# Kernel optimization log

Measured on AMD Instinct MI355X. Metric: run time of the kernel, lower is better.

The kernel has to match this reference:

```python
import jax, jax.numpy as jnp
import numpy as np

B, S, D = 2, 4096, 2048
H, DK = 16, 128          # num_heads, head_dim (DK == DV)
GATE_NORM = 16.0         # gate_logit_normalizer (GLA default)


def setup_inputs() -> dict:
    key = jax.random.key(0)
    ks = jax.random.split(key, 6)
    sc = 1.0 / np.sqrt(D)
    return {
        "x": jax.random.normal(ks[0], (B, S, D), dtype=jnp.float32),
        "Wq": jax.random.normal(ks[1], (D, D), dtype=jnp.float32) * sc,
        "Wk": jax.random.normal(ks[2], (D, D), dtype=jnp.float32) * sc,
        "Wv": jax.random.normal(ks[3], (D, D), dtype=jnp.float32) * sc,
        "Wg": jax.random.normal(ks[4], (D, D), dtype=jnp.float32) * sc,
        "Wo": jax.random.normal(ks[5], (D, D), dtype=jnp.float32) * sc,
    }


def _gla(q, k, v, gk):
    """Gated linear attention recurrence.
    q,k,gk: [B,H,S,DK]; v: [B,H,S,DV]. Returns o: [B,H,S,DV].
    S_t = diag(exp(gk_t)) @ S_{t-1} + k_t v_t^T;  o_t = q_t @ S_t.
    """
    def step(state, inp):
        q_t, k_t, v_t, g_t = inp  # each [B,H,DK] / [B,H,DV]
        state = state * jnp.exp(g_t)[..., None] + k_t[..., None] * v_t[..., None, :]
        o_t = jnp.einsum("bhk,bhkv->bhv", q_t, state)
        return state, o_t

    init = jnp.zeros((q.shape[0], q.shape[1], q.shape[3], v.shape[3]), q.dtype)
    # scan over time: move seq axis to front
    xs = tuple(jnp.moveaxis(t, 2, 0) for t in (q, k, v, gk))
    _, o = jax.lax.scan(step, init, xs)  # o: [S,B,H,DV]
    return jnp.moveaxis(o, 0, 2)


def reference(x, Wq, Wk, Wv, Wg, Wo):
    b, s, _ = x.shape
    split = lambda t: t.reshape(b, s, H, DK).transpose(0, 2, 1, 3)  # [B,H,S,DK]
    q = split(x @ Wq) * (DK ** -0.5)
    k = split(x @ Wk)
    v = split(x @ Wv)
    gk = jax.nn.log_sigmoid(split(x @ Wg)) / GATE_NORM  # data-dependent log decay
    o = _gla(q, k, v, gk)                                # [B,H,S,DV]
    o = o.transpose(0, 2, 1, 3).reshape(b, s, H * DK)
    return o @ Wo
```

## Files before the change

### kernel.cpp

```cpp
#include <hip/hip_runtime.h>
#include <hip/hip_bf16.h>

#define B_SZ 2
#define S_LEN 4096
#define D_MODEL 2048
#define NH 16
#define DKH 128
#define CHUNK 32
#define SEG 256
#define NSEG 16
#define NCH 8
#define GEMM_M 8192
#define GEMM_N 2048
#define GEMM_K 2048
#define NKT 32

typedef __bf16 bf16x8 __attribute__((ext_vector_type(8)));
typedef float f32x4 __attribute__((ext_vector_type(4)));
typedef unsigned short u16x4 __attribute__((ext_vector_type(4)));
typedef unsigned short u16x8 __attribute__((ext_vector_type(8)));

__device__ inline float bf2f(unsigned short u) {
  unsigned int x = ((unsigned int)u) << 16;
  return __builtin_bit_cast(float, x);
}
__device__ inline unsigned short f2bf(float f) {
  __hip_bfloat16 h = __float2bfloat16(f);
  return __builtin_bit_cast(unsigned short, h);
}
__device__ inline unsigned int packhl(float s) {
  unsigned short h = f2bf(s);
  unsigned short l = f2bf(s - bf2f(h));
  return ((unsigned int)h << 16) | (unsigned int)l;
}

__global__ __launch_bounds__(256) void cast_bf16_kernel(const float* __restrict__ in,
                                                        unsigned short* __restrict__ out,
                                                        int nvec8) {
  int i = blockIdx.x * 256 + threadIdx.x;
  if (i >= nvec8) return;
  const float4* p = (const float4*)in + (size_t)i * 2;
  float4 a = p[0], b = p[1];
  uint4 o;
  o.x = (unsigned)f2bf(a.x) | ((unsigned)f2bf(a.y) << 16);
  o.y = (unsigned)f2bf(a.z) | ((unsigned)f2bf(a.w) << 16);
  o.z = (unsigned)f2bf(b.x) | ((unsigned)f2bf(b.y) << 16);
  o.w = (unsigned)f2bf(b.z) | ((unsigned)f2bf(b.w) << 16);
  ((uint4*)out)[i] = o;
}

__global__ __launch_bounds__(256) void transpose_cast_kernel(const float* __restrict__ W,
                                                             unsigned short* __restrict__ Wt) {
  __shared__ float tile[64][65];
  const int n0 = blockIdx.x * 64, k0 = blockIdx.y * 64;
  for (int jj = 0; jj < 16; ++jj) {
    int flat = threadIdx.x + jj * 256;
    int r = flat >> 6, c = flat & 63;
    tile[r][c] = W[(size_t)(k0 + r) * D_MODEL + n0 + c];
  }
  __syncthreads();
  for (int jj = 0; jj < 16; ++jj) {
    int flat = threadIdx.x + jj * 256;
    int rr = flat >> 6, cc = flat & 63;
    Wt[(size_t)(n0 + rr) * D_MODEL + k0 + cc] = f2bf(tile[cc][rr]);
  }
}

__device__ __forceinline__ void async16(void* lds_dst, const void* gsrc) {
  __builtin_amdgcn_global_load_lds((__attribute__((address_space(1))) void*)(void*)gsrc,
                                   (__attribute__((address_space(3))) void*)lds_dst,
                                   16, 0, 0);
}

__device__ __forceinline__ void memfence_compiler() { asm volatile("" ::: "memory"); }

__device__ __forceinline__ void stage_tile(const unsigned short* __restrict__ G,
                                           int row0, int k0,
                                           unsigned short* lds_buf, int tid) {
  const int r = tid >> 3;
  const int ssw = ((tid & 7) ^ (r & 7)) * 8;
  const unsigned short* src = &G[(size_t)(row0 + r) * GEMM_K + k0 + ssw];
  char* dst = (char*)lds_buf + (tid >> 6) * 1024;
#pragma unroll
  for (int j = 0; j < 4; ++j)
    async16(dst + j * 8192, src + (size_t)j * 64 * GEMM_K);
}

template <int MODE>
__global__ __launch_bounds__(512, 2) void gemm256(const unsigned short* __restrict__ A,
                                                  const unsigned short* __restrict__ Bt,
                                                  void* __restrict__ Cout) {
  __shared__ unsigned short As[2][256 * 64];
  __shared__ unsigned short Bs[2][256 * 64];
  const int tid = threadIdx.x;
  const int lane = tid & 63;
  const int wid = tid >> 6;
  const int wm = wid >> 2, wn = wid & 3;
  const int lr = lane & 15, lg = lane >> 4;

  const int lid = blockIdx.y * 8 + blockIdx.x;
  const int swz = (lid & 7) * 32 + (lid >> 3);
  const int bm = (swz >> 3) * 256;
  const int bn = (swz & 7) * 256;

  f32x4 acc[8][4] = {};

  stage_tile(A, bm, 0, As[0], tid);
  stage_tile(Bt, bn, 0, Bs[0], tid);
  stage_tile(A, bm, 64, As[1], tid);
  stage_tile(Bt, bn, 64, Bs[1], tid);
  asm volatile("s_waitcnt vmcnt(8)" ::: "memory");
  __builtin_amdgcn_s_barrier();
  __builtin_amdgcn_sched_barrier(0);
  memfence_compiler();

  for (int t = 0; t < NKT; ++t) {
    const int cur = t & 1;
    const unsigned short* Ac = As[cur];
    const unsigned short* Bc = Bs[cur];
#pragma unroll
    for (int ks = 0; ks < 2; ++ks) {
      bf16x8 av[8], bv[4];
      const int slot = ((ks << 2) | lg) ^ (lr & 7);
#pragma unroll
      for (int mi = 0; mi < 8; ++mi)
        av[mi] = *(const bf16x8*)&Ac[(wm * 128 + mi * 16 + lr) * 64 + slot * 8];
#pragma unroll
      for (int nj = 0; nj < 4; ++nj)
        bv[nj] = *(const bf16x8*)&Bc[(wn * 64 + nj * 16 + lr) * 64 + slot * 8];
      __builtin_amdgcn_s_setprio(1);
#pragma unroll
      for (int mi = 0; mi < 8; ++mi)
#pragma unroll
        for (int nj = 0; nj < 4; ++nj)
          acc[mi][nj] = __builtin_amdgcn_mfma_f32_16x16x32_bf16(av[mi], bv[nj], acc[mi][nj], 0, 0, 0);
      __builtin_amdgcn_s_setprio(0);
    }
    memfence_compiler();
    __builtin_amdgcn_s_barrier();
    __builtin_amdgcn_sched_barrier(0);
    if (t + 2 < NKT) {
      stage_tile(A, bm, (t + 2) * 64, As[cur], tid);
      stage_tile(Bt, bn, (t + 2) * 64, Bs[cur], tid);
      asm volatile("s_waitcnt vmcnt(8)" ::: "memory");
    } else {
      asm volatile("s_waitcnt vmcnt(0)" ::: "memory");
    }
    __builtin_amdgcn_s_barrier();
    __builtin_amdgcn_sched_barrier(0);
    memfence_compiler();
  }

#pragma unroll
  for (int mi = 0; mi < 8; ++mi) {
#pragma unroll
    for (int nj = 0; nj < 4; ++nj) {
#pragma unroll
      for (int r = 0; r < 4; ++r) {
        int row = bm + wm * 128 + mi * 16 + lg * 4 + r;
        int col = bn + wn * 64 + nj * 16 + lr;
        float v = acc[mi][nj][r];
        size_t idx = (size_t)row * GEMM_N + col;
        if constexpr (MODE == 0) {
          ((unsigned short*)Cout)[idx] = f2bf(v);
        } else if constexpr (MODE == 1) {
          ((unsigned short*)Cout)[idx] = f2bf(v * 0.08838834764831845f);
        } else if constexpr (MODE == 2) {
          float ls = fminf(v, 0.f) - log1pf(expf(-fabsf(v)));
          ((unsigned short*)Cout)[idx] = f2bf(ls * 0.0625f);
        } else {
          ((float*)Cout)[idx] = v;
        }
      }
    }
  }
}

__global__ __launch_bounds__(256) void gla_seg1(
    const unsigned short* qb, const unsigned short* __restrict__ kb,
    const unsigned short* __restrict__ vb, const unsigned short* __restrict__ gkb,
    unsigned short* qhat, unsigned short* __restrict__ obuf,
    float* __restrict__ dS, float* __restrict__ Dseg) {
  __shared__ __align__(16) unsigned short rawq[32 * 128];
  __shared__ __align__(16) unsigned short rawk[32 * 128];
  __shared__ __align__(16) unsigned short rawv[32 * 128];
  __shared__ __align__(16) unsigned short rawg[32 * 128];
  __shared__ __align__(16) unsigned short qt[32 * 136];
  __shared__ __align__(16) unsigned short kt[32 * 136];
  __shared__ __align__(16) unsigned short ktT[128 * 40];
  __shared__ __align__(16) unsigned short vT[128 * 40];
  __shared__ __align__(16) unsigned short Am[32 * 40];
  __shared__ __align__(16) unsigned short Shi[128 * 136];
  __shared__ __align__(16) unsigned short Slo[128 * 136];
  __shared__ __align__(16) float EGC[128];

  const int tid = threadIdx.x;
  const int lane = tid & 63, w = tid >> 6;
  const int lr = lane & 15, lg = lane >> 4;
  const int seg = blockIdx.x, h = blockIdx.y, b = blockIdx.z;
  const int colQ = h * DKH;
  const size_t segtok = (size_t)b * S_LEN + (size_t)seg * SEG;

  f32x4 sacc[2][8] = {};
  float gseg = 0.f;

  auto stage_chunk = [&](int c) {
    const size_t ctok = segtok + c * CHUNK;
    const int r0 = 8 * w;
    const int rr = r0 + (lane >> 4);
    const int cc = (lane & 15) * 8;
    async16(&rawq[(r0) * 128], &qb[(ctok + rr) * D_MODEL + colQ + cc]);
    async16(&rawq[(r0 + 4) * 128], &qb[(ctok + rr + 4) * D_MODEL + colQ + cc]);
    async16(&rawk[(r0) * 128], &kb[(ctok + rr) * D_MODEL + colQ + cc]);
    async16(&rawk[(r0 + 4) * 128], &kb[(ctok + rr + 4) * D_MODEL + colQ + cc]);
    async16(&rawv[(r0) * 128], &vb[(ctok + rr) * D_MODEL + colQ + cc]);
    async16(&rawv[(r0 + 4) * 128], &vb[(ctok + rr + 4) * D_MODEL + colQ + cc]);
    async16(&rawg[(r0) * 128], &gkb[(ctok + rr) * D_MODEL + colQ + cc]);
    async16(&rawg[(r0 + 4) * 128], &gkb[(ctok + rr + 4) * D_MODEL + colQ + cc]);
  };

  stage_chunk(0);

  for (int c = 0; c < NCH; ++c) {
    const size_t ctok = segtok + c * CHUNK;
    __syncthreads();

#pragma unroll
    for (int ktl = 0; ktl < 2; ++ktl) {
      const int k0 = 32 * w + ktl * 16 + lg * 4;
#pragma unroll
      for (int vt = 0; vt < 8; ++vt) {
        const int v = vt * 16 + lr;
        u16x4 hv, lv;
#pragma unroll
        for (int r = 0; r < 4; ++r) {
          float s = sacc[ktl][vt][r];
          unsigned short h_ = f2bf(s);
          hv[r] = h_;
          lv[r] = f2bf(s - bf2f(h_));
        }
        *(u16x4*)&Shi[v * 136 + k0] = hv;
        *(u16x4*)&Slo[v * 136 + k0] = lv;
      }
    }

    if (tid < 128) {
      const int k = tid;
      float g = 0.f;
      const float egsp = __expf(gseg);
#pragma unroll
      for (int t = 0; t < CHUNK; ++t) {
        g += bf2f(rawg[t * 128 + k]);
        float eg = __expf(g), ieg = __expf(-g);
        float qv = bf2f(rawq[t * 128 + k]) * eg;
        qt[t * 136 + k] = f2bf(qv);
        qhat[(ctok + t) * D_MODEL + colQ + k] = f2bf(qv * egsp);
        unsigned short kbf = f2bf(bf2f(rawk[t * 128 + k]) * ieg);
        kt[t * 136 + k] = kbf;
        ktT[k * 40 + t] = kbf;
      }
      EGC[k] = __expf(g);
      gseg += g;
    } else {
      const int j = tid - 128;
#pragma unroll
      for (int i = 0; i < 4; ++i) {
        int f = j * 4 + i;
        int t = f >> 4, v0 = (f & 15) * 8;
        u16x8 r8 = *(const u16x8*)&rawv[t * 128 + v0];
#pragma unroll
        for (int e = 0; e < 8; ++e) vT[(v0 + e) * 40 + t] = r8[e];
      }
    }
    __syncthreads();

    if (c + 1 < NCH) stage_chunk(c + 1);

    {
      const int tt = w >> 1, tpt = w & 1;
      if (tpt <= tt) {
        f32x4 aacc = {};
#pragma unroll
        for (int ks = 0; ks < 4; ++ks) {
          bf16x8 qa = *(const bf16x8*)&qt[(tt * 16 + lr) * 136 + ks * 32 + lg * 8];
          bf16x8 ka = *(const bf16x8*)&kt[(tpt * 16 + lr) * 136 + ks * 32 + lg * 8];
          aacc = __builtin_amdgcn_mfma_f32_16x16x32_bf16(qa, ka, aacc, 0, 0, 0);
        }
#pragma unroll
        for (int r = 0; r < 4; ++r) {
          int t = tt * 16 + lg * 4 + r;
          int tp = tpt * 16 + lr;
          Am[t * 40 + tp] = f2bf((tp <= t) ? aacc[r] : 0.f);
        }
      } else {
#pragma unroll
        for (int r = 0; r < 4; ++r) Am[(lg * 4 + r) * 40 + 16 + lr] = 0;
      }
    }
    __syncthreads();

    f32x4 oacc[2][2] = {};
#pragma unroll
    for (int ks = 0; ks < 4; ++ks) {
      bf16x8 qa0 = *(const bf16x8*)&qt[(lr) * 136 + ks * 32 + lg * 8];
      bf16x8 qa1 = *(const bf16x8*)&qt[(16 + lr) * 136 + ks * 32 + lg * 8];
#pragma unroll
      for (int vtl = 0; vtl < 2; ++vtl) {
        const int v = (2 * w + vtl) * 16 + lr;
        bf16x8 bh = *(const bf16x8*)&Shi[v * 136 + ks * 32 + lg * 8];
        bf16x8 bl = *(const bf16x8*)&Slo[v * 136 + ks * 32 + lg * 8];
        oacc[0][vtl] = __builtin_amdgcn_mfma_f32_16x16x32_bf16(qa0, bh, oacc[0][vtl], 0, 0, 0);
        oacc[0][vtl] = __builtin_amdgcn_mfma_f32_16x16x32_bf16(qa0, bl, oacc[0][vtl], 0, 0, 0);
        oacc[1][vtl] = __builtin_amdgcn_mfma_f32_16x16x32_bf16(qa1, bh, oacc[1][vtl], 0, 0, 0);
        oacc[1][vtl] = __builtin_amdgcn_mfma_f32_16x16x32_bf16(qa1, bl, oacc[1][vtl], 0, 0, 0);
      }
    }
    {
      bf16x8 am0 = *(const bf16x8*)&Am[(lr) * 40 + lg * 8];
      bf16x8 am1 = *(const bf16x8*)&Am[(16 + lr) * 40 + lg * 8];
#pragma unroll
      for (int vtl = 0; vtl < 2; ++vtl) {
        const int v = (2 * w + vtl) * 16 + lr;
        bf16x8 bv = *(const bf16x8*)&vT[v * 40 + lg * 8];
        oacc[0][vtl] = __builtin_amdgcn_mfma_f32_16x16x32_bf16(am0, bv, oacc[0][vtl], 0, 0, 0);
        oacc[1][vtl] = __builtin_amdgcn_mfma_f32_16x16x32_bf16(am1, bv, oacc[1][vtl], 0, 0, 0);
      }
    }
#pragma unroll
    for (int tt = 0; tt < 2; ++tt)
#pragma unroll
      for (int vtl = 0; vtl < 2; ++vtl) {
        const int v = (2 * w + vtl) * 16 + lr;
#pragma unroll
        for (int r = 0; r < 4; ++r)
          obuf[(ctok + tt * 16 + lg * 4 + r) * D_MODEL + colQ + v] = f2bf(oacc[tt][vtl][r]);
      }
    {
      bf16x8 ak0 = *(const bf16x8*)&ktT[(32 * w + lr) * 40 + lg * 8];
      bf16x8 ak1 = *(const bf16x8*)&ktT[(32 * w + 16 + lr) * 40 + lg * 8];
#pragma unroll
      for (int vt = 0; vt < 8; ++vt) {
        bf16x8 bv = *(const bf16x8*)&vT[(vt * 16 + lr) * 40 + lg * 8];
        sacc[0][vt] = __builtin_amdgcn_mfma_f32_16x16x32_bf16(ak0, bv, sacc[0][vt], 0, 0, 0);
        sacc[1][vt] = __builtin_amdgcn_mfma_f32_16x16x32_bf16(ak1, bv, sacc[1][vt], 0, 0, 0);
      }
      f32x4 eg0 = *(const f32x4*)&EGC[32 * w + lg * 4];
      f32x4 eg1 = *(const f32x4*)&EGC[32 * w + 16 + lg * 4];
#pragma unroll
      for (int vt = 0; vt < 8; ++vt) {
        sacc[0][vt] *= eg0;
        sacc[1][vt] *= eg1;
      }
    }
  }

  const size_t dsbase = (((size_t)(b * NH + h) * NSEG + seg) * 128) * 128;
#pragma unroll
  for (int ktl = 0; ktl < 2; ++ktl) {
    const int k0 = 32 * w + ktl * 16 + lg * 4;
#pragma unroll
    for (int vt = 0; vt < 8; ++vt) {
      const int v = vt * 16 + lr;
      float4 st;
      st.x = sacc[ktl][vt][0]; st.y = sacc[ktl][vt][1];
      st.z = sacc[ktl][vt][2]; st.w = sacc[ktl][vt][3];
      *(float4*)&dS[dsbase + (size_t)v * 128 + k0] = st;
    }
  }
  if (tid < 128) Dseg[((size_t)(b * NH + h) * NSEG + seg) * 128 + tid] = __expf(gseg);
}

__global__ __launch_bounds__(256) void gla_scan(float* dS, const float* __restrict__ Dseg) {
  unsigned int* Spk = (unsigned int*)dS;
  const int tid = threadIdx.x;
  const int vs = blockIdx.x, h = blockIdx.y, b = blockIdx.z;
  const int v = vs * 16 + (tid >> 4);
  const int k0 = (tid & 15) * 8;
  const size_t bh = (size_t)b * NH + h;
  float s[8];
#pragma unroll
  for (int j = 0; j < 8; ++j) s[j] = 0.f;

  for (int sg = 0; sg < NSEG; ++sg) {
    const size_t base = ((bh * NSEG + sg) * 128 + v) * 128 + k0;
    float4 x0 = *(const float4*)&dS[base];
    float4 x1 = *(const float4*)&dS[base + 4];
    const size_t dbase = (bh * NSEG + sg) * 128 + k0;
    float4 d0 = *(const float4*)&Dseg[dbase];
    float4 d1 = *(const float4*)&Dseg[dbase + 4];

    uint4 p0, p1;
    p0.x = packhl(s[0]); p0.y = packhl(s[1]); p0.z = packhl(s[2]); p0.w = packhl(s[3]);
    p1.x = packhl(s[4]); p1.y = packhl(s[5]); p1.z = packhl(s[6]); p1.w = packhl(s[7]);
    *(uint4*)&Spk[base] = p0;
    *(uint4*)&Spk[base + 4] = p1;

    s[0] = d0.x * s[0] + x0.x; s[1] = d0.y * s[1] + x0.y;
    s[2] = d0.z * s[2] + x0.z; s[3] = d0.w * s[3] + x0.w;
    s[4] = d1.x * s[4] + x1.x; s[5] = d1.y * s[5] + x1.y;
    s[6] = d1.z * s[6] + x1.z; s[7] = d1.w * s[7] + x1.w;
  }
}

__global__ __launch_bounds__(256) void gla_corr(const unsigned short* __restrict__ qhat,
                                                const unsigned int* __restrict__ Spk,
                                                unsigned short* __restrict__ obuf) {
  __shared__ __align__(16) unsigned short Sh[128 * 136];
  __shared__ __align__(16) unsigned short Sl[128 * 136];
  const int tid = threadIdx.x;
  const int lane = tid & 63, w = tid >> 6;
  const int lr = lane & 15, lg = lane >> 4;
  const int seg = blockIdx.x, h = blockIdx.y, b = blockIdx.z;
  const int colQ = h * DKH;
  const size_t segtok = (size_t)b * S_LEN + (size_t)seg * SEG;
  const size_t sbase = (((size_t)(b * NH + h) * NSEG + seg) * 128) * 128;

#pragma unroll
  for (int i = 0; i < 16; ++i) {
    int f = tid + i * 256;
    int v = f >> 5, k0 = (f & 31) * 4;
    uint4 p = *(const uint4*)&Spk[sbase + (size_t)v * 128 + k0];
    u16x4 hv, lv;
    hv[0] = (unsigned short)(p.x >> 16); lv[0] = (unsigned short)(p.x & 0xffff);
    hv[1] = (unsigned short)(p.y >> 16); lv[1] = (unsigned short)(p.y & 0xffff);
    hv[2] = (unsigned short)(p.z >> 16); lv[2] = (unsigned short)(p.z & 0xffff);
    hv[3] = (unsigned short)(p.w >> 16); lv[3] = (unsigned short)(p.w & 0xffff);
    *(u16x4*)&Sh[v * 136 + k0] = hv;
    *(u16x4*)&Sl[v * 136 + k0] = lv;
  }
  __syncthreads();

  for (int nt = 0; nt < 4; ++nt) {
    const int ttile = w * 4 + nt;
    const int t = ttile * 16 + lr;
    f32x4 acc8[8];
#pragma unroll
    for (int vt = 0; vt < 8; ++vt) {
      u16x4 c4 = *(const u16x4*)&obuf[(segtok + t) * D_MODEL + colQ + vt * 16 + lg * 4];
      acc8[vt][0] = bf2f(c4[0]); acc8[vt][1] = bf2f(c4[1]);
      acc8[vt][2] = bf2f(c4[2]); acc8[vt][3] = bf2f(c4[3]);
    }
#pragma unroll
    for (int ks = 0; ks < 4; ++ks) {
      bf16x8 bq = *(const bf16x8*)&qhat[(segtok + t) * D_MODEL + colQ + ks * 32 + lg * 8];
#pragma unroll
      for (int vt = 0; vt < 8; ++vt) {
        bf16x8 ah = *(const bf16x8*)&Sh[(vt * 16 + lr) * 136 + ks * 32 + lg * 8];
        bf16x8 al = *(const bf16x8*)&Sl[(vt * 16 + lr) * 136 + ks * 32 + lg * 8];
        acc8[vt] = __builtin_amdgcn_mfma_f32_16x16x32_bf16(ah, bq, acc8[vt], 0, 0, 0);
        acc8[vt] = __builtin_amdgcn_mfma_f32_16x16x32_bf16(al, bq, acc8[vt], 0, 0, 0);
      }
    }
#pragma unroll
    for (int vt = 0; vt < 8; ++vt) {
      u16x4 pk;
#pragma unroll
      for (int r = 0; r < 4; ++r) pk[r] = f2bf(acc8[vt][r]);
      *(u16x4*)&obuf[(segtok + t) * D_MODEL + colQ + vt * 16 + lg * 4] = pk;
    }
  }
}

extern "C" void kernel_launch(void* const* d_in, const int* in_sizes, int n_in,
                              void* d_out, int out_size, void* d_ws, size_t ws_size,
                              hipStream_t stream) {
  const float* x = (const float*)d_in[0];
  const float* W[5] = {(const float*)d_in[1], (const float*)d_in[2], (const float*)d_in[3],
                       (const float*)d_in[4], (const float*)d_in[5]};
  float* out = (float*)d_out;
  char* ws = (char*)d_ws;

  const size_t XBN = (size_t)B_SZ * S_LEN * D_MODEL;
  const size_t DD = (size_t)D_MODEL * D_MODEL;
  const size_t NSTATE = (size_t)B_SZ * NH * NSEG * 128 * 128;

  size_t off = 0;
  unsigned short* xb = (unsigned short*)(ws + off); off += XBN * 2;
  unsigned short* Wt = (unsigned short*)(ws + off); off += 5 * DD * 2;
  unsigned short* qb = (unsigned short*)(ws + off); off += XBN * 2;
  unsigned short* kb = (unsigned short*)(ws + off); off += XBN * 2;
  unsigned short* vb = (unsigned short*)(ws + off); off += XBN * 2;
  unsigned short* gkb = (unsigned short*)(ws + off); off += XBN * 2;
  float* dS = (float*)(ws + off); off += NSTATE * 4;
  float* Dsg = (float*)(ws + off); off += (size_t)B_SZ * NH * NSEG * 128 * 4;
  unsigned short* obuf = xb;

  cast_bf16_kernel<<<dim3((unsigned)(XBN / 8 / 256)), dim3(256), 0, stream>>>(x, xb, (int)(XBN / 8));
  for (int i = 0; i < 5; ++i)
    transpose_cast_kernel<<<dim3(32, 32), dim3(256), 0, stream>>>(W[i], Wt + (size_t)i * DD);

  dim3 gg(GEMM_N / 256, GEMM_M / 256);
  gemm256<1><<<gg, 512, 0, stream>>>(xb, Wt + 0 * DD, (void*)qb);
  gemm256<0><<<gg, 512, 0, stream>>>(xb, Wt + 1 * DD, (void*)kb);
  gemm256<0><<<gg, 512, 0, stream>>>(xb, Wt + 2 * DD, (void*)vb);
  gemm256<2><<<gg, 512, 0, stream>>>(xb, Wt + 3 * DD, (void*)gkb);

  gla_seg1<<<dim3(NSEG, NH, B_SZ), 256, 0, stream>>>(qb, kb, vb, gkb, qb , obuf, dS, Dsg);
  gla_scan<<<dim3(8, NH, B_SZ), 256, 0, stream>>>(dS, Dsg);
  gla_corr<<<dim3(NSEG, NH, B_SZ), 256, 0, stream>>>(qb , (const unsigned int*)dS, obuf);

  gemm256<3><<<gg, 512, 0, stream>>>(obuf, Wt + 4 * DD, (void*)out);
}
```

Before: 704.2 us.

## Split GEMM k-step into four quadrant phases interleaving half-tile async loads

Restructures the 256x256 bf16 GEMM main loop into four MFMA phases over 4x2 sub-quadrants. Global-to-LDS loads are split into 128-row halves issued between phases, so the next tile's loads overlap the MFMA work instead of being issued all at once after compute. This is an 8-wave ping-pong style schedule meant to hide memory latency and reduce the stall at each barrier. In exchange it adds more barriers per iteration and relies on delicate vmcnt accounting across the half-tile stages.

```diff
diff --git a/kernel.cpp b/kernel.cpp
--- a/kernel.cpp
+++ b/kernel.cpp
@@ -71,19 +71,20 @@
                                    (__attribute__((address_space(3))) void*)lds_dst,
                                    16, 0, 0);
 }
-
 __device__ __forceinline__ void memfence_compiler() { asm volatile("" ::: "memory"); }
-
-__device__ __forceinline__ void stage_tile(const unsigned short* __restrict__ G,
+#define BAR()  __builtin_amdgcn_s_barrier()
+#define SCHB() __builtin_amdgcn_sched_barrier(0)
+#define LGK0() asm volatile("s_waitcnt lgkmcnt(0)" ::: "memory")
+
+__device__ __forceinline__ void stage_half(const unsigned short* __restrict__ G,
                                            int row0, int k0,
-                                           unsigned short* lds_buf, int tid) {
+                                           unsigned short* lds_half, int tid) {
   const int r = tid >> 3;
   const int ssw = ((tid & 7) ^ (r & 7)) * 8;
   const unsigned short* src = &G[(size_t)(row0 + r) * GEMM_K + k0 + ssw];
-  char* dst = (char*)lds_buf + (tid >> 6) * 1024;
-#pragma unroll
-  for (int j = 0; j < 4; ++j)
-    async16(dst + j * 8192, src + (size_t)j * 64 * GEMM_K);
+  char* dst = (char*)lds_half + (tid >> 6) * 1024;
+  async16(dst, src);
+  async16(dst + 8192, src + (size_t)64 * GEMM_K);
 }
 
 template <int MODE>
@@ -105,49 +106,104 @@
 
   f32x4 acc[8][4] = {};
 
-  stage_tile(A, bm, 0, As[0], tid);
-  stage_tile(Bt, bn, 0, Bs[0], tid);
-  stage_tile(A, bm, 64, As[1], tid);
-  stage_tile(Bt, bn, 64, Bs[1], tid);
-  asm volatile("s_waitcnt vmcnt(8)" ::: "memory");
-  __builtin_amdgcn_s_barrier();
-  __builtin_amdgcn_sched_barrier(0);
-  memfence_compiler();
+  stage_half(A, bm, 0, &As[0][0], tid);
+  stage_half(A, bm + 128, 0, &As[0][8192], tid);
+  stage_half(Bt, bn, 0, &Bs[0][0], tid);
+  stage_half(Bt, bn + 128, 0, &Bs[0][8192], tid);
+  stage_half(A, bm, 64, &As[1][0], tid);
+  stage_half(Bt, bn, 64, &Bs[1][0], tid);
+  stage_half(Bt, bn + 128, 64, &Bs[1][8192], tid);
+  asm volatile("s_waitcnt vmcnt(6)" ::: "memory");
+  BAR(); SCHB();
 
   for (int t = 0; t < NKT; ++t) {
     const int cur = t & 1;
     const unsigned short* Ac = As[cur];
     const unsigned short* Bc = Bs[cur];
+    bf16x8 av0[4][2], av1[4][2], bv0[2][2], bv1[2][2];
+
 #pragma unroll
     for (int ks = 0; ks < 2; ++ks) {
-      bf16x8 av[8], bv[4];
       const int slot = ((ks << 2) | lg) ^ (lr & 7);
 #pragma unroll
-      for (int mi = 0; mi < 8; ++mi)
-        av[mi] = *(const bf16x8*)&Ac[(wm * 128 + mi * 16 + lr) * 64 + slot * 8];
-#pragma unroll
-      for (int nj = 0; nj < 4; ++nj)
-        bv[nj] = *(const bf16x8*)&Bc[(wn * 64 + nj * 16 + lr) * 64 + slot * 8];
-      __builtin_amdgcn_s_setprio(1);
-#pragma unroll
-      for (int mi = 0; mi < 8; ++mi)
-#pragma unroll
-        for (int nj = 0; nj < 4; ++nj)
-          acc[mi][nj] = __builtin_amdgcn_mfma_f32_16x16x32_bf16(av[mi], bv[nj], acc[mi][nj], 0, 0, 0);
-      __builtin_amdgcn_s_setprio(0);
-    }
-    memfence_compiler();
-    __builtin_amdgcn_s_barrier();
-    __builtin_amdgcn_sched_barrier(0);
+      for (int mi = 0; mi < 4; ++mi)
+        av0[mi][ks] = *(const bf16x8*)&Ac[(wm * 128 + mi * 16 + lr) * 64 + slot * 8];
+#pragma unroll
+      for (int nj = 0; nj < 2; ++nj)
+        bv0[nj][ks] = *(const bf16x8*)&Bc[(wn * 64 + nj * 16 + lr) * 64 + slot * 8];
+    }
+    if (t + 1 < NKT) stage_half(A, bm + 128, (t + 1) * 64, &As[cur ^ 1][8192], tid);
+    BAR(); LGK0(); SCHB();
+    __builtin_amdgcn_s_setprio(1);
+#pragma unroll
+    for (int ks = 0; ks < 2; ++ks)
+#pragma unroll
+      for (int mi = 0; mi < 4; ++mi)
+#pragma unroll
+        for (int nj = 0; nj < 2; ++nj)
+          acc[mi][nj] = __builtin_amdgcn_mfma_f32_16x16x32_bf16(av0[mi][ks], bv0[nj][ks], acc[mi][nj], 0, 0, 0);
+    __builtin_amdgcn_s_setprio(0);
+    BAR(); SCHB();
+
+#pragma unroll
+    for (int ks = 0; ks < 2; ++ks) {
+      const int slot = ((ks << 2) | lg) ^ (lr & 7);
+#pragma unroll
+      for (int nj = 0; nj < 2; ++nj)
+        bv1[nj][ks] = *(const bf16x8*)&Bc[(wn * 64 + (2 + nj) * 16 + lr) * 64 + slot * 8];
+    }
+    BAR(); LGK0(); SCHB();
+    __builtin_amdgcn_s_setprio(1);
+#pragma unroll
+    for (int ks = 0; ks < 2; ++ks)
+#pragma unroll
+      for (int mi = 0; mi < 4; ++mi)
+#pragma unroll
+        for (int nj = 0; nj < 2; ++nj)
+          acc[mi][2 + nj] = __builtin_amdgcn_mfma_f32_16x16x32_bf16(av0[mi][ks], bv1[nj][ks], acc[mi][2 + nj], 0, 0, 0);
+    __builtin_amdgcn_s_setprio(0);
+    BAR(); SCHB();
+
+#pragma unroll
+    for (int ks = 0; ks < 2; ++ks) {
+      const int slot = ((ks << 2) | lg) ^ (lr & 7);
+#pragma unroll
+      for (int mi = 0; mi < 4; ++mi)
+        av1[mi][ks] = *(const bf16x8*)&Ac[(wm * 128 + (4 + mi) * 16 + lr) * 64 + slot * 8];
+    }
+    if (t + 2 < NKT) stage_half(Bt, bn, (t + 2) * 64, &Bs[cur][0], tid);
+    BAR(); LGK0(); SCHB();
+    __builtin_amdgcn_s_setprio(1);
+#pragma unroll
+    for (int ks = 0; ks < 2; ++ks)
+#pragma unroll
+      for (int mi = 0; mi < 4; ++mi)
+#pragma unroll
+        for (int nj = 0; nj < 2; ++nj)
+          acc[4 + mi][nj] = __builtin_amdgcn_mfma_f32_16x16x32_bf16(av1[mi][ks], bv0[nj][ks], acc[4 + mi][nj], 0, 0, 0);
+    __builtin_amdgcn_s_setprio(0);
+    BAR(); SCHB();
+
     if (t + 2 < NKT) {
-      stage_tile(A, bm, (t + 2) * 64, As[cur], tid);
-      stage_tile(Bt, bn, (t + 2) * 64, Bs[cur], tid);
-      asm volatile("s_waitcnt vmcnt(8)" ::: "memory");
-    } else {
+      stage_half(Bt, bn + 128, (t + 2) * 64, &Bs[cur][8192], tid);
+      stage_half(A, bm, (t + 2) * 64, &As[cur][0], tid);
+    }
+    BAR(); SCHB();
+    __builtin_amdgcn_s_setprio(1);
+#pragma unroll
+    for (int ks = 0; ks < 2; ++ks)
+#pragma unroll
+      for (int mi = 0; mi < 4; ++mi)
+#pragma unroll
+        for (int nj = 0; nj < 2; ++nj)
+          acc[4 + mi][2 + nj] = __builtin_amdgcn_mfma_f32_16x16x32_bf16(av1[mi][ks], bv1[nj][ks], acc[4 + mi][2 + nj], 0, 0, 0);
+    __builtin_amdgcn_s_setprio(0);
+    if (t < NKT - 2) {
+      asm volatile("s_waitcnt vmcnt(6)" ::: "memory");
+    } else if (t == NKT - 2) {
       asm volatile("s_waitcnt vmcnt(0)" ::: "memory");
     }
-    __builtin_amdgcn_s_barrier();
-    __builtin_amdgcn_sched_barrier(0);
+    BAR(); SCHB();
     memfence_compiler();
   }
 
```

After: 709.9 us. About the same (+0.8%).
